# Optimization experiments

Hardware: AMD Instinct MI355X
Metric: run time of the kernel (lower is better)

Reference implementation:

```python
import jax, jax.numpy as jnp
import numpy as np

VOCAB = 4000
U = 30000   # unique tokens
M = 12      # max mid-char length
H = 256     # hidden_size
O = 768     # output_size
B = 16      # sequences
L = 2048    # tokens per sequence (equal lengths -> jit-friendly reassemble)


def setup_inputs() -> dict:
    key = jax.random.key(0)
    ks = jax.random.split(key, 8)
    emb_table = jax.random.normal(ks[0], (VOCAB, H), dtype=jnp.float32)
    emb_table = emb_table.at[0].set(0.0)  # padding_idx=0
    head_w = jax.random.normal(ks[1], (3 * H, O), dtype=jnp.float32) * 0.02
    head_b = jax.random.normal(ks[2], (O,), dtype=jnp.float32) * 0.02
    first = jax.random.randint(ks[3], (U,), 0, VOCAB, dtype=jnp.int32)
    mid = jax.random.randint(ks[4], (U, M), 0, VOCAB, dtype=jnp.int32)
    last = jax.random.randint(ks[5], (U,), 0, VOCAB, dtype=jnp.int32)
    inv_i = jax.random.randint(ks[6], (B * L,), 0, U, dtype=jnp.int32)
    return {"emb_table": emb_table, "head_w": head_w, "head_b": head_b,
            "first": first, "mid": mid, "last": last, "inv_i": inv_i,
            "batch": B, "seq_len": L}


def reference(emb_table, head_w, head_b, first, mid, last, inv_i, batch, seq_len):
    def lookup(ids):
        # emulate padding_idx=0: id 0 contributes a zero vector
        v = emb_table[ids]
        return v * (ids != 0)[..., None].astype(v.dtype)

    rep = jnp.concatenate(
        [lookup(first), lookup(mid).sum(axis=1), lookup(last)], axis=-1)  # [U, 3H]
    out = rep @ head_w + head_b                                           # [U, O]
    tok = out[inv_i].reshape(batch, seq_len, -1)                          # [B, L, O]
    # reassemble: one zero row before and after each sequence (F.pad (1,1) on time)
    return jnp.pad(tok, ((0, 0), (1, 1), (0, 0)))                         # [B, L+2, O]
```

## Files before the change

kernel.cpp:

```cpp
#include <hip/hip_runtime.h>

#define VOCAB 4000
#define UNIQ 30000
#define MIDN 12
#define HID 256
#define OUT 768
#define BATCH 16
#define SEQ 2048

#define NXCD 8
#define XCOLS 96
#define SUBC 16
#define NSUB 48
#define TCHUNK 2048
#define NCHUNK 16
#define TPASS 256
#define NPASS 8
#define PLANE 32008

typedef __attribute__((ext_vector_type(8))) short short8;
typedef __attribute__((ext_vector_type(4))) float f32x4;

__device__ __forceinline__ float bitsf(unsigned int x) {
    float f; __builtin_memcpy(&f, &x, 4); return f;
}
__device__ __forceinline__ unsigned short f2bf(float f) {
    unsigned int x;
    __builtin_memcpy(&x, &f, 4);
    x += 0x7fff + ((x >> 16) & 1);
    return (unsigned short)(x >> 16);
}

__global__ __launch_bounds__(256) void build_idsT(
    const int* __restrict__ first, const int* __restrict__ mid,
    const int* __restrict__ last, const int* __restrict__ inv_i,
    short* __restrict__ idsT)
{
    int t = blockIdx.x * 256 + threadIdx.x;
    if (t >= BATCH * SEQ) return;
    int u = inv_i[t];
    int4 m0 = *reinterpret_cast<const int4*>(&mid[u * MIDN]);
    int4 m1 = *reinterpret_cast<const int4*>(&mid[u * MIDN + 4]);
    int4 m2 = *reinterpret_cast<const int4*>(&mid[u * MIDN + 8]);
    short ids[16];
    ids[0]  = (short)first[u];
    ids[1]  = (short)m0.x; ids[2]  = (short)m0.y; ids[3]  = (short)m0.z; ids[4]  = (short)m0.w;
    ids[5]  = (short)m1.x; ids[6]  = (short)m1.y; ids[7]  = (short)m1.z; ids[8]  = (short)m1.w;
    ids[9]  = (short)m2.x; ids[10] = (short)m2.y; ids[11] = (short)m2.z; ids[12] = (short)m2.w;
    ids[13] = (short)last[u];
    ids[14] = 0; ids[15] = 0;
    *reinterpret_cast<short8*>(&idsT[(size_t)t * 16])     = *reinterpret_cast<short8*>(&ids[0]);
    *reinterpret_cast<short8*>(&idsT[(size_t)t * 16 + 8]) = *reinterpret_cast<short8*>(&ids[8]);
}

__global__ __launch_bounds__(256) void conv_w(
    const float* __restrict__ W, unsigned short* __restrict__ Wt)
{
    __shared__ float T[32][33];
    const int s  = blockIdx.z;
    const int n0 = blockIdx.x * 32;
    const int h0 = blockIdx.y * 32;
    const int tx = threadIdx.x & 31;
    const int ty = threadIdx.x >> 5;

    #pragma unroll
    for (int k = 0; k < 4; ++k) {
        int h = ty + 8 * k;
        T[h][tx] = W[(size_t)(s * HID + h0 + h) * OUT + n0 + tx];
    }
    __syncthreads();
    #pragma unroll
    for (int k = 0; k < 4; ++k) {
        int n = ty + 8 * k;
        Wt[(size_t)(s * OUT + n0 + n) * HID + h0 + tx] = f2bf(T[tx][n]);
    }
}

__global__ __launch_bounds__(256) void proj_mfma(
    const float* __restrict__ E,
    const unsigned short* __restrict__ Wt,
    unsigned short* __restrict__ P,
    unsigned short* __restrict__ Pmid)
{
    const int s  = blockIdx.z;
    const int n0 = blockIdx.x * 128;
    const int m0 = blockIdx.y * 128;
    const unsigned short* Wts = Wt + (size_t)s * OUT * HID;

    __shared__ short As[128][40];
    __shared__ short Bs[128][40];

    const int tid  = threadIdx.x;
    const int lane = tid & 63;
    const int w    = tid >> 6;
    const int wm   = w >> 1;
    const int wn   = w & 1;
    const int lo   = lane & 15;
    const int hi   = lane >> 4;

    f32x4 acc[4][4] = {};

    for (int kt = 0; kt < HID; kt += 32) {
        #pragma unroll
        for (int p = 0; p < 2; ++p) {
            int idx = p * 256 + tid;
            int row = idx >> 2;
            int ko  = (idx & 3) * 8;
            int gm  = m0 + row;
            f32x4 e0 = {}, e1 = {};
            if (gm < VOCAB) {
                e0 = *reinterpret_cast<const f32x4*>(&E[(size_t)gm * HID + kt + ko]);
                e1 = *reinterpret_cast<const f32x4*>(&E[(size_t)gm * HID + kt + ko + 4]);
            }
            short8 v;
            v[0] = (short)f2bf(e0.x); v[1] = (short)f2bf(e0.y);
            v[2] = (short)f2bf(e0.z); v[3] = (short)f2bf(e0.w);
            v[4] = (short)f2bf(e1.x); v[5] = (short)f2bf(e1.y);
            v[6] = (short)f2bf(e1.z); v[7] = (short)f2bf(e1.w);
            *reinterpret_cast<short8*>(&As[row][ko]) = v;
        }
        #pragma unroll
        for (int p = 0; p < 2; ++p) {
            int idx = p * 256 + tid;
            int col = idx >> 2;
            int ko  = (idx & 3) * 8;
            short8 v = *reinterpret_cast<const short8*>(
                &Wts[(size_t)(n0 + col) * HID + kt + ko]);
            *reinterpret_cast<short8*>(&Bs[col][ko]) = v;
        }
        __syncthreads();

        short8 a[4], b[4];
        #pragma unroll
        for (int f = 0; f < 4; ++f)
            a[f] = *reinterpret_cast<short8*>(&As[wm * 64 + f * 16 + lo][hi * 8]);
        #pragma unroll
        for (int f = 0; f < 4; ++f)
            b[f] = *reinterpret_cast<short8*>(&Bs[wn * 64 + f * 16 + lo][hi * 8]);
        #pragma unroll
        for (int fm = 0; fm < 4; ++fm)
            #pragma unroll
            for (int fn = 0; fn < 4; ++fn)
                acc[fm][fn] = __builtin_amdgcn_mfma_f32_16x16x32_bf16(
                    a[fm], b[fn], acc[fm][fn], 0, 0, 0);
        __syncthreads();
    }

    #pragma unroll
    for (int fm = 0; fm < 4; ++fm) {
        #pragma unroll
        for (int fn = 0; fn < 4; ++fn) {
            #pragma unroll
            for (int r = 0; r < 4; ++r) {
                int gm = m0 + wm * 64 + fm * 16 + hi * 4 + r;
                int gn = n0 + wn * 64 + fn * 16 + lo;
                if (gm < VOCAB) {
                    unsigned short val = f2bf(acc[fm][fn][r]);
                    unsigned int sl = (unsigned int)gn / XCOLS;
                    unsigned int cc = (unsigned int)gn - sl * XCOLS;
                    P[((size_t)(sl * 3 + s) * VOCAB + gm) * XCOLS + cc] = val;
                    if (s == 1) {
                        Pmid[((size_t)(gn >> 4) * VOCAB + gm) * SUBC + (gn & 15)] = val;
                    }
                }
            }
        }
    }
}

extern __shared__ char lds_raw[];

__global__ __launch_bounds__(1024) void token_lds(
    const unsigned short* __restrict__ P,
    const unsigned short* __restrict__ Pmid,
    const short* __restrict__ idsT,
    const float* __restrict__ bias,
    float* __restrict__ out)
{
    const int bid   = blockIdx.x;
    const int xcd   = bid & 7;
    const int r     = bid >> 3;
    const int s6    = r % 6;
    const int chunk = r / 6;
    const int sub   = xcd * 6 + s6;

    const int tid = threadIdx.x;
    const int l4  = tid & 3;
    const int grp = tid >> 2;
    const int lane = tid & 63;
    const int gbase = lane & ~3;

    {
        const unsigned short* src = Pmid + (size_t)sub * VOCAB * SUBC;
        #pragma unroll
        for (int i = 0; i < 16; ++i) {
            int idx = i * 1024 + tid;
            if (idx < VOCAB * 4) {
                int row = idx >> 2;
                int q   = idx & 3;
                uint2 v = *reinterpret_cast<const uint2*>(&src[row * SUBC + q * 4]);
                *reinterpret_cast<uint2*>(lds_raw + q * PLANE + row * 8) = v;
            }
        }
    }
    __syncthreads();

    char* myplane = lds_raw + l4 * PLANE;

    const int csub = s6 * SUBC + l4 * 4;
    const int colc = xcd * XCOLS + csub;
    const unsigned short* P0 = P + (size_t)xcd * 3 * VOCAB * XCOLS + csub;
    const unsigned short* P2 = P0 + (size_t)2 * VOCAB * XCOLS;

    const f32x4 bv = *reinterpret_cast<const f32x4*>(&bias[colc]);

    const int t0 = chunk * TCHUNK + grp;
    uint2 idv = *reinterpret_cast<const uint2*>(&idsT[(size_t)t0 * 16 + l4 * 4]);

    #pragma unroll 1
    for (int p = 0; p < NPASS; ++p) {
        const int t = t0 + p * TPASS;

        unsigned int w[8];
        #pragma unroll
        for (int s = 0; s < 4; ++s) {
            w[2 * s]     = __shfl(idv.x, gbase + s, 64);
            w[2 * s + 1] = __shfl(idv.y, gbase + s, 64);
        }
        const int fid = (int)(w[0] & 0xffffu);
        const int lid = (int)(w[6] >> 16);

        uint2 fv = *reinterpret_cast<const uint2*>(&P0[(size_t)fid * XCOLS]);
        uint2 lv = *reinterpret_cast<const uint2*>(&P2[(size_t)lid * XCOLS]);
        if (p + 1 < NPASS)
            idv = *reinterpret_cast<const uint2*>(
                &idsT[(size_t)(t + TPASS) * 16 + l4 * 4]);

        uint2 mv[MIDN];
        #pragma unroll
        for (int m = 0; m < MIDN; ++m) {
            int k = m + 1;
            int rid = (int)((w[k >> 1] >> ((k & 1) * 16)) & 0xffffu);
            mv[m] = *reinterpret_cast<const uint2*>(myplane + rid * 8);
        }

        float a0 = bv.x, a1 = bv.y, a2 = bv.z, a3 = bv.w;
        #pragma unroll
        for (int m = 0; m < MIDN; ++m) {
            a0 += bitsf(mv[m].x << 16);
            a1 += bitsf(mv[m].x & 0xffff0000u);
            a2 += bitsf(mv[m].y << 16);
            a3 += bitsf(mv[m].y & 0xffff0000u);
        }
        a0 += bitsf(fv.x << 16); a1 += bitsf(fv.x & 0xffff0000u);
        a2 += bitsf(fv.y << 16); a3 += bitsf(fv.y & 0xffff0000u);
        a0 += bitsf(lv.x << 16); a1 += bitsf(lv.x & 0xffff0000u);
        a2 += bitsf(lv.y << 16); a3 += bitsf(lv.y & 0xffff0000u);

        const int b = t >> 11;
        const int l = t & (SEQ - 1);
        float* dst = &out[((size_t)(b * (SEQ + 2) + l + 1)) * OUT + colc];
        f32x4 o = {a0, a1, a2, a3};
        __builtin_nontemporal_store(o, reinterpret_cast<f32x4*>(dst));
    }
}

__global__ void zero_pads(float* __restrict__ out)
{
    int j = blockIdx.x * blockDim.x + threadIdx.x;
    const int n4 = OUT / 4;
    if (j >= BATCH * 2 * n4) return;
    int b  = j / (2 * n4);
    int r  = (j / n4) & 1;
    int c4 = j % n4;
    int row = r ? (SEQ + 1) : 0;
    f32x4 z = {};
    *reinterpret_cast<f32x4*>(
        &out[((size_t)(b * (SEQ + 2) + row)) * OUT + c4 * 4]) = z;
}

extern "C" void kernel_launch(void* const* d_in, const int* in_sizes, int n_in,
                              void* d_out, int out_size, void* d_ws, size_t ws_size,
                              hipStream_t stream)
{
    const float* emb    = (const float*)d_in[0];
    const float* head_w = (const float*)d_in[1];
    const float* head_b = (const float*)d_in[2];
    const int*   first  = (const int*)d_in[3];
    const int*   mid    = (const int*)d_in[4];
    const int*   last   = (const int*)d_in[5];
    const int*   inv_i  = (const int*)d_in[6];
    float* out = (float*)d_out;

    char* ws = (char*)d_ws;
    unsigned short* P    = (unsigned short*)ws;
    unsigned short* Wt   = (unsigned short*)(ws + 18432000);
    unsigned short* Pmid = (unsigned short*)(ws + 19611648);
    short*          idsT = (short*)(ws + 25755648);

    build_idsT<<<(BATCH * SEQ + 255) / 256, 256, 0, stream>>>(
        first, mid, last, inv_i, idsT);

    dim3 gw(OUT / 32, HID / 32, 3);
    conv_w<<<gw, 256, 0, stream>>>(head_w, Wt);

    dim3 g1(OUT / 128, (VOCAB + 127) / 128, 3);
    proj_mfma<<<g1, 256, 0, stream>>>(emb, Wt, P, Pmid);

    token_lds<<<NCHUNK * 6 * NXCD, 1024, 4 * PLANE, stream>>>(
        P, Pmid, idsT, head_b, out);

    const int pad4 = BATCH * 2 * (OUT / 4);
    zero_pads<<<(pad4 + 255) / 256, 256, 0, stream>>>(out);
}
```

Before: 70.38 us.

## Make token kernel persistent with software-pipelined id loads and gathers

The token kernel now launches 256 blocks that each handle three (column-slice, chunk) tasks, so the LDS table for the mid projection is reloaded only when the slice changes. Ids are loaded as full 32-byte rows per thread and double-buffered, replacing the per-pass shuffles. The first/last gathers are prefetched one pass ahead. The projection kernel also stops writing the unused mid plane into P, which shrinks that buffer and the writes. This trades more registers and a fully unrolled loop for fewer LDS fills and more overlap of latency.

New measurement: 67.11 us. 4.6% less time.

```diff
diff --git a/kernel.cpp b/kernel.cpp
--- a/kernel.cpp
+++ b/kernel.cpp
@@ -11,7 +11,6 @@
 #define NXCD 8
 #define XCOLS 96
 #define SUBC 16
-#define NSUB 48
 #define TCHUNK 2048
 #define NCHUNK 16
 #define TPASS 256
@@ -20,6 +19,8 @@
 
 typedef __attribute__((ext_vector_type(8))) short short8;
 typedef __attribute__((ext_vector_type(4))) float f32x4;
+typedef __attribute__((ext_vector_type(4))) unsigned int u32x4;
+typedef __attribute__((ext_vector_type(2))) unsigned int u32x2;
 
 __device__ __forceinline__ float bitsf(unsigned int x) {
     float f; __builtin_memcpy(&f, &x, 4); return f;
@@ -156,11 +157,13 @@
                 int gn = n0 + wn * 64 + fn * 16 + lo;
                 if (gm < VOCAB) {
                     unsigned short val = f2bf(acc[fm][fn][r]);
-                    unsigned int sl = (unsigned int)gn / XCOLS;
-                    unsigned int cc = (unsigned int)gn - sl * XCOLS;
-                    P[((size_t)(sl * 3 + s) * VOCAB + gm) * XCOLS + cc] = val;
                     if (s == 1) {
                         Pmid[((size_t)(gn >> 4) * VOCAB + gm) * SUBC + (gn & 15)] = val;
+                    } else {
+                        int so = (s == 0) ? 0 : 1;
+                        unsigned int sl = (unsigned int)gn / XCOLS;
+                        unsigned int cc = (unsigned int)gn - sl * XCOLS;
+                        P[(((size_t)sl * 2 + so) * VOCAB + gm) * XCOLS + cc] = val;
                     }
                 }
             }
@@ -177,91 +180,125 @@
     const float* __restrict__ bias,
     float* __restrict__ out)
 {
-    const int bid   = blockIdx.x;
-    const int xcd   = bid & 7;
-    const int r     = bid >> 3;
-    const int s6    = r % 6;
-    const int chunk = r / 6;
-    const int sub   = xcd * 6 + s6;
+    const int xcd = blockIdx.x & 7;
+    const int bi  = blockIdx.x >> 3;
 
     const int tid = threadIdx.x;
     const int l4  = tid & 3;
     const int grp = tid >> 2;
-    const int lane = tid & 63;
-    const int gbase = lane & ~3;
-
-    {
-        const unsigned short* src = Pmid + (size_t)sub * VOCAB * SUBC;
-        #pragma unroll
-        for (int i = 0; i < 16; ++i) {
-            int idx = i * 1024 + tid;
-            if (idx < VOCAB * 4) {
-                int row = idx >> 2;
-                int q   = idx & 3;
-                uint2 v = *reinterpret_cast<const uint2*>(&src[row * SUBC + q * 4]);
-                *reinterpret_cast<uint2*>(lds_raw + q * PLANE + row * 8) = v;
-            }
-        }
-    }
-    __syncthreads();
 
     char* myplane = lds_raw + l4 * PLANE;
-
-    const int csub = s6 * SUBC + l4 * 4;
-    const int colc = xcd * XCOLS + csub;
-    const unsigned short* P0 = P + (size_t)xcd * 3 * VOCAB * XCOLS + csub;
-    const unsigned short* P2 = P0 + (size_t)2 * VOCAB * XCOLS;
-
-    const f32x4 bv = *reinterpret_cast<const f32x4*>(&bias[colc]);
-
-    const int t0 = chunk * TCHUNK + grp;
-    uint2 idv = *reinterpret_cast<const uint2*>(&idsT[(size_t)t0 * 16 + l4 * 4]);
+    const unsigned short* Pbase = P + (size_t)xcd * 2 * VOCAB * XCOLS;
+
+    int cur_sl = -1;
 
     #pragma unroll 1
-    for (int p = 0; p < NPASS; ++p) {
-        const int t = t0 + p * TPASS;
-
-        unsigned int w[8];
-        #pragma unroll
-        for (int s = 0; s < 4; ++s) {
-            w[2 * s]     = __shfl(idv.x, gbase + s, 64);
-            w[2 * s + 1] = __shfl(idv.y, gbase + s, 64);
-        }
-        const int fid = (int)(w[0] & 0xffffu);
-        const int lid = (int)(w[6] >> 16);
-
-        uint2 fv = *reinterpret_cast<const uint2*>(&P0[(size_t)fid * XCOLS]);
-        uint2 lv = *reinterpret_cast<const uint2*>(&P2[(size_t)lid * XCOLS]);
-        if (p + 1 < NPASS)
-            idv = *reinterpret_cast<const uint2*>(
-                &idsT[(size_t)(t + TPASS) * 16 + l4 * 4]);
-
-        uint2 mv[MIDN];
-        #pragma unroll
-        for (int m = 0; m < MIDN; ++m) {
-            int k = m + 1;
-            int rid = (int)((w[k >> 1] >> ((k & 1) * 16)) & 0xffffu);
-            mv[m] = *reinterpret_cast<const uint2*>(myplane + rid * 8);
-        }
-
-        float a0 = bv.x, a1 = bv.y, a2 = bv.z, a3 = bv.w;
-        #pragma unroll
-        for (int m = 0; m < MIDN; ++m) {
-            a0 += bitsf(mv[m].x << 16);
-            a1 += bitsf(mv[m].x & 0xffff0000u);
-            a2 += bitsf(mv[m].y << 16);
-            a3 += bitsf(mv[m].y & 0xffff0000u);
-        }
-        a0 += bitsf(fv.x << 16); a1 += bitsf(fv.x & 0xffff0000u);
-        a2 += bitsf(fv.y << 16); a3 += bitsf(fv.y & 0xffff0000u);
-        a0 += bitsf(lv.x << 16); a1 += bitsf(lv.x & 0xffff0000u);
-        a2 += bitsf(lv.y << 16); a3 += bitsf(lv.y & 0xffff0000u);
-
-        const int b = t >> 11;
-        const int l = t & (SEQ - 1);
-        float* dst = &out[((size_t)(b * (SEQ + 2) + l + 1)) * OUT + colc];
-        f32x4 o = {a0, a1, a2, a3};
-        __builtin_nontemporal_store(o, reinterpret_cast<f32x4*>(dst));
+    for (int k = 0; k < 3; ++k) {
+        const int task = bi * 3 + k;
+        const int sl   = task >> 4;
+        const int ch   = task & 15;
+
+        if (sl != cur_sl) {
+            if (cur_sl >= 0) __syncthreads();
+            const int sub = xcd * 6 + sl;
+            const unsigned short* src = Pmid + (size_t)sub * VOCAB * SUBC;
+            #pragma unroll
+            for (int i = 0; i < 16; ++i) {
+                int idx = i * 1024 + tid;
+                if (idx < VOCAB * 4) {
+                    int row = idx >> 2;
+                    int q   = idx & 3;
+                    uint2 v = *reinterpret_cast<const uint2*>(&src[row * SUBC + q * 4]);
+                    *reinterpret_cast<uint2*>(lds_raw + q * PLANE + row * 8) = v;
+                }
+            }
+            __syncthreads();
+            cur_sl = sl;
+        }
+
+        const int csub = sl * SUBC + l4 * 4;
+        const int colc = xcd * XCOLS + csub;
+        const unsigned short* P0 = Pbase + csub;
+        const unsigned short* P2 = Pbase + (size_t)VOCAB * XCOLS + csub;
+        const f32x4 bv = *reinterpret_cast<const f32x4*>(&bias[colc]);
+
+        const int t0 = ch * TCHUNK + grp;
+
+#define LDIDS(lo_, hi_, tt_) { \
+        const u32x4* _r = reinterpret_cast<const u32x4*>(&idsT[(size_t)(tt_) * 16]); \
+        lo_ = _r[0]; hi_ = _r[1]; }
+
+#define GATHER(fv_, lv_, lo_, hi_) { \
+        int _fid = (int)((lo_).x & 0xffffu); \
+        int _lid = (int)((hi_).z >> 16); \
+        fv_ = *reinterpret_cast<const uint2*>(&P0[(size_t)_fid * XCOLS]); \
+        lv_ = *reinterpret_cast<const uint2*>(&P2[(size_t)_lid * XCOLS]); }
+
+        u32x4 ilA, ihA, ilB, ihB;
+        uint2 fvA, lvA, fvB, lvB;
+
+        LDIDS(ilA, ihA, t0);
+        LDIDS(ilB, ihB, t0 + TPASS);
+        GATHER(fvA, lvA, ilA, ihA);
+
+        #pragma unroll
+        for (int p = 0; p < NPASS; ++p) {
+            const bool even = (p & 1) == 0;
+            u32x4 clo = even ? ilA : ilB;
+            u32x4 chi = even ? ihA : ihB;
+            uint2 cfv = even ? fvA : fvB;
+            uint2 clv = even ? lvA : lvB;
+
+            if (p + 1 < NPASS) {
+                if (even) { GATHER(fvB, lvB, ilB, ihB); }
+                else      { GATHER(fvA, lvA, ilA, ihA); }
+            }
+            if (p + 2 < NPASS) {
+                if (even) { LDIDS(ilA, ihA, t0 + (p + 2) * TPASS); }
+                else      { LDIDS(ilB, ihB, t0 + (p + 2) * TPASS); }
+            }
+
+            int rid[MIDN];
+            rid[0]  = (int)(clo.x >> 16);
+            rid[1]  = (int)(clo.y & 0xffffu);
+            rid[2]  = (int)(clo.y >> 16);
+            rid[3]  = (int)(clo.z & 0xffffu);
+            rid[4]  = (int)(clo.z >> 16);
+            rid[5]  = (int)(clo.w & 0xffffu);
+            rid[6]  = (int)(clo.w >> 16);
+            rid[7]  = (int)(chi.x & 0xffffu);
+            rid[8]  = (int)(chi.x >> 16);
+            rid[9]  = (int)(chi.y & 0xffffu);
+            rid[10] = (int)(chi.y >> 16);
+            rid[11] = (int)(chi.z & 0xffffu);
+
+            uint2 mv[MIDN];
+            #pragma unroll
+            for (int m = 0; m < MIDN; ++m)
+                mv[m] = *reinterpret_cast<const uint2*>(myplane + rid[m] * 8);
+
+            float a0 = bv.x, a1 = bv.y, a2 = bv.z, a3 = bv.w;
+            #pragma unroll
+            for (int m = 0; m < MIDN; ++m) {
+                a0 += bitsf(mv[m].x << 16);
+                a1 += bitsf(mv[m].x & 0xffff0000u);
+                a2 += bitsf(mv[m].y << 16);
+                a3 += bitsf(mv[m].y & 0xffff0000u);
+            }
+            a0 += bitsf(cfv.x << 16); a1 += bitsf(cfv.x & 0xffff0000u);
+            a2 += bitsf(cfv.y << 16); a3 += bitsf(cfv.y & 0xffff0000u);
+            a0 += bitsf(clv.x << 16); a1 += bitsf(clv.x & 0xffff0000u);
+            a2 += bitsf(clv.y << 16); a3 += bitsf(clv.y & 0xffff0000u);
+
+            const int t = t0 + p * TPASS;
+            const int b = t >> 11;
+            const int l = t & (SEQ - 1);
+            float* dst = &out[((size_t)(b * (SEQ + 2) + l + 1)) * OUT + colc];
+            f32x4 o = {a0, a1, a2, a3};
+            __builtin_nontemporal_store(o, reinterpret_cast<f32x4*>(dst));
+        }
+#undef LDIDS
+#undef GATHER
     }
 }
 
@@ -294,9 +331,9 @@
 
     char* ws = (char*)d_ws;
     unsigned short* P    = (unsigned short*)ws;
-    unsigned short* Wt   = (unsigned short*)(ws + 18432000);
-    unsigned short* Pmid = (unsigned short*)(ws + 19611648);
-    short*          idsT = (short*)(ws + 25755648);
+    unsigned short* Wt   = (unsigned short*)(ws + 12288000);
+    unsigned short* Pmid = (unsigned short*)(ws + 13467648);
+    short*          idsT = (short*)(ws + 19611648);
 
     build_idsT<<<(BATCH * SEQ + 255) / 256, 256, 0, stream>>>(
         first, mid, last, inv_i, idsT);
@@ -307,8 +344,7 @@
     dim3 g1(OUT / 128, (VOCAB + 127) / 128, 3);
     proj_mfma<<<g1, 256, 0, stream>>>(emb, Wt, P, Pmid);
 
-    token_lds<<<NCHUNK * 6 * NXCD, 1024, 4 * PLANE, stream>>>(
-        P, Pmid, idsT, head_b, out);
+    token_lds<<<256, 1024, 4 * PLANE, stream>>>(P, Pmid, idsT, head_b, out);
 
     const int pad4 = BATCH * 2 * (OUT / 4);
     zero_pads<<<(pad4 + 255) / 256, 256, 0, stream>>>(out);
```
